# Kernel optimization log

Measured on AMD Instinct MI355X. Metric: run time of the kernel, lower is better.

The kernel has to match this reference:

```python
import jax, jax.numpy as jnp
import numpy as np

NUM_LANDMARKS = 256
PINV_ITERS = 6


def iterative_inv(K):
    # Newton-Schulz iterative pseudo-inverse (Nystromformer), K: [B, m, m]
    I = jnp.eye(K.shape[-1], dtype=K.dtype)
    V = K.swapaxes(-1, -2) / (jnp.max(jnp.sum(K, axis=-2)) * jnp.max(jnp.sum(K, axis=-1)))
    for _ in range(PINV_ITERS):
        KV = K @ V
        V = 0.25 * V @ (13.0 * I - KV @ (15.0 * I - KV @ (7.0 * I - KV)))
    return V


def nystrom_attention_matrix(q, k, m):
    # q, k: [B, N, d] -> approximate softmax(q k^T / sqrt(d)) of shape [B, N, N]
    B, N, d = q.shape
    scale = 1.0 / jnp.sqrt(jnp.asarray(d, q.dtype))
    L = N // m
    q_l = q.reshape(B, m, L, d).mean(axis=2)  # landmark queries [B, m, d]
    k_l = k.reshape(B, m, L, d).mean(axis=2)  # landmark keys    [B, m, d]
    k1 = jax.nn.softmax(jnp.einsum('bnd,bmd->bnm', q, k_l) * scale, axis=-1)   # [B, N, m]
    k2 = jax.nn.softmax(jnp.einsum('bld,bmd->blm', q_l, k_l) * scale, axis=-1) # [B, m, m]
    k3 = jax.nn.softmax(jnp.einsum('bmd,bnd->bmn', q_l, k) * scale, axis=-1)   # [B, m, N]
    return (k1 @ iterative_inv(k2)) @ k3  # [B, N, N]


def setup_inputs() -> dict:
    key = jax.random.key(0)
    ks = jax.random.split(key, 8)
    B, C, T, W, H = 2, 64, 4, 32, 32
    d = C // 8
    scale = 0.05  # keep q.k scores in a sane softmax range
    return {
        'x': jax.random.normal(ks[0], (B, C, T, W, H), dtype=jnp.float32),
        'wq': jax.random.normal(ks[1], (d, C), dtype=jnp.float32) * scale,
        'bq': jax.random.normal(ks[2], (d,), dtype=jnp.float32) * scale,
        'wk': jax.random.normal(ks[3], (d, C), dtype=jnp.float32) * scale,
        'bk': jax.random.normal(ks[4], (d,), dtype=jnp.float32) * scale,
        'wv': jax.random.normal(ks[5], (C, C), dtype=jnp.float32) * scale,
        'bv': jax.random.normal(ks[6], (C,), dtype=jnp.float32) * scale,
        'gamma': jax.random.normal(ks[7], (1,), dtype=jnp.float32),
    }


def reference(x, wq, bq, wk, bk, wv, bv, gamma):
    B, C, T, W, H = x.shape
    N = T * W * H
    xf = x.reshape(B, C, N)
    # 1x1x1 Conv3d == per-token linear over channels
    q = jnp.einsum('oc,bcn->bno', wq, xf) + bq            # [B, N, C//8]
    k = jnp.einsum('oc,bcn->bno', wk, xf) + bk            # [B, N, C//8]
    v = jnp.einsum('oc,bcn->bon', wv, xf) + bv[None, :, None]  # [B, C, N]
    attn = nystrom_attention_matrix(q, k, NUM_LANDMARKS)  # [B, N, N]
    # out = bmm(value, attn^T): out[b,c,i] = sum_j v[b,c,j] * attn[b,i,j]
    out = jnp.einsum('bcj,bij->bci', v, attn).reshape(B, C, T, W, H)
    out = gamma[0] * out + x
    return out, attn
```

## Files before the change

### kernel.cpp

```cpp
#include <hip/hip_runtime.h>
#include <hip/hip_bf16.h>
#include <math.h>

#define NB 2
#define NC 64
#define ND 8
#define NN 4096
#define NM 256
#define NL 16
#define SCALE 0.35355339059327373f

typedef __attribute__((ext_vector_type(4))) float f32x4;
typedef __attribute__((ext_vector_type(8))) short bf16x8;

__device__ inline ushort f2bf(float f) {
  __hip_bfloat16 h = __float2bfloat16(f);
  return *reinterpret_cast<ushort*>(&h);
}
__device__ inline float bf2f(ushort u) {
  return __uint_as_float(((unsigned int)u) << 16);
}

__device__ inline void gl_lds16(const void* g, void* l) {
  __builtin_amdgcn_global_load_lds(
      (const __attribute__((address_space(1))) unsigned int*)g,
      (__attribute__((address_space(3))) unsigned int*)l, 16, 0, 0);
}

__global__ __launch_bounds__(256) void qkv4_kernel(
    const float* __restrict__ x,
    const float* __restrict__ wq, const float* __restrict__ bq,
    const float* __restrict__ wk, const float* __restrict__ bk,
    const float* __restrict__ wv, const float* __restrict__ bv,
    float* __restrict__ q, float* __restrict__ k, float* __restrict__ v,
    float* __restrict__ ql, float* __restrict__ kl) {
  __shared__ float ws[4][NC];
  int o0 = blockIdx.x * 4;
  int b = blockIdx.z;
  int n0 = blockIdx.y * 1024;
  int t = threadIdx.x;
  {
    int j = t >> 6, c = t & 63;
    int o = o0 + j;
    const float* wrow;
    if (o < ND)          wrow = wq + (size_t)o * NC;
    else if (o < 2 * ND) wrow = wk + (size_t)(o - ND) * NC;
    else                 wrow = wv + (size_t)(o - 2 * ND) * NC;
    ws[j][c] = wrow[c];
  }
  __syncthreads();
  int n = n0 + t * 4;
  float4 acc[4];
  #pragma unroll
  for (int j = 0; j < 4; ++j) {
    int o = o0 + j;
    float bias = (o < ND) ? bq[o] : (o < 2 * ND ? bk[o - ND] : bv[o - 2 * ND]);
    acc[j].x = bias; acc[j].y = bias; acc[j].z = bias; acc[j].w = bias;
  }
  for (int c = 0; c < NC; ++c) {
    float4 xv = *(const float4*)(x + ((size_t)b * NC + c) * NN + n);
    #pragma unroll
    for (int j = 0; j < 4; ++j) {
      float wc = ws[j][c];
      acc[j].x += wc * xv.x; acc[j].y += wc * xv.y;
      acc[j].z += wc * xv.z; acc[j].w += wc * xv.w;
    }
  }
  #pragma unroll
  for (int j = 0; j < 4; ++j) {
    int o = o0 + j;
    if (o < ND) {
      float* qp = q + ((size_t)b * NN + n) * ND + o;
      qp[0] = acc[j].x; qp[8] = acc[j].y; qp[16] = acc[j].z; qp[24] = acc[j].w;
    } else if (o < 2 * ND) {
      float* kp = k + ((size_t)b * NN + n) * ND + (o - ND);
      kp[0] = acc[j].x; kp[8] = acc[j].y; kp[16] = acc[j].z; kp[24] = acc[j].w;
    } else {
      *(float4*)(v + ((size_t)b * NC + (o - 2 * ND)) * NN + n) = acc[j];
    }
    if (o < 2 * ND) {
      float s4 = acc[j].x + acc[j].y + acc[j].z + acc[j].w;
      s4 += __shfl_xor(s4, 1);
      s4 += __shfl_xor(s4, 2);
      if ((t & 3) == 0) {
        int g = n0 / 16 + (t >> 2);
        float* dst = (o < ND) ? ql : kl;
        dst[((size_t)b * NM + g) * ND + (o & 7)] = s4 * (1.0f / 16.0f);
      }
    }
  }
}

__global__ __launch_bounds__(256) void scores_all_kernel(
    const float* __restrict__ q, const float* __restrict__ ql,
    const float* __restrict__ kw, const float* __restrict__ kl,
    ushort* __restrict__ k1bf, float* __restrict__ k2w,
    ushort* __restrict__ k3bf) {
  __shared__ float skl[NM][9];
  __shared__ float wred[4], wsum[4];
  int blk = blockIdx.x;
  int t = threadIdx.x;
  if (blk < 2048 + 128) {
    const float* Q; int R, b, xrow;
    bool isbf;
    if (blk < 2048) { b = blk >> 10; xrow = blk & 1023; Q = q;  R = NN; isbf = true; }
    else { int r = blk - 2048; b = r >> 6; xrow = r & 63; Q = ql; R = NM; isbf = false; }
    for (int i = t; i < NM * ND; i += 256) skl[i >> 3][i & 7] = kl[(size_t)b * NM * ND + i];
    __syncthreads();
    int wave = t >> 6, lane = t & 63;
    int r = xrow * 4 + wave;
    const float* qrow = Q + ((size_t)b * R + r) * ND;
    float qr[ND];
    #pragma unroll
    for (int dd = 0; dd < ND; ++dd) qr[dd] = qrow[dd];
    float sc[4];
    float lmax = -1e30f;
    #pragma unroll
    for (int s = 0; s < 4; ++s) {
      int j = lane + 64 * s;
      float a = 0.f;
      #pragma unroll
      for (int dd = 0; dd < ND; ++dd) a += qr[dd] * skl[j][dd];
      sc[s] = a * SCALE;
      lmax = fmaxf(lmax, sc[s]);
    }
    for (int off = 32; off; off >>= 1) lmax = fmaxf(lmax, __shfl_xor(lmax, off));
    float lsum = 0.f;
    #pragma unroll
    for (int s = 0; s < 4; ++s) { sc[s] = expf(sc[s] - lmax); lsum += sc[s]; }
    for (int off = 32; off; off >>= 1) lsum += __shfl_xor(lsum, off);
    float inv = 1.0f / lsum;
    if (isbf) {
      #pragma unroll
      for (int s = 0; s < 4; ++s)
        k1bf[((size_t)b * R + r) * NM + lane + 64 * s] = f2bf(sc[s] * inv);
    } else {
      #pragma unroll
      for (int s = 0; s < 4; ++s)
        k2w[((size_t)b * R + r) * NM + lane + 64 * s] = sc[s] * inv;
    }
  } else {
    int r = blk - 2176;
    int b = r >> 8, i = r & 255;
    float qr[ND];
    #pragma unroll
    for (int dd = 0; dd < ND; ++dd) qr[dd] = ql[((size_t)b * NM + i) * ND + dd];
    float sc[16];
    float lmax = -1e30f;
    #pragma unroll
    for (int s = 0; s < 16; ++s) {
      int n = t + 256 * s;
      const float* kp = kw + ((size_t)b * NN + n) * ND;
      float a = 0.f;
      #pragma unroll
      for (int dd = 0; dd < ND; ++dd) a += qr[dd] * kp[dd];
      sc[s] = a * SCALE;
      lmax = fmaxf(lmax, sc[s]);
    }
    for (int off = 32; off; off >>= 1) lmax = fmaxf(lmax, __shfl_xor(lmax, off));
    if ((t & 63) == 0) wred[t >> 6] = lmax;
    __syncthreads();
    lmax = fmaxf(fmaxf(wred[0], wred[1]), fmaxf(wred[2], wred[3]));
    float lsum = 0.f;
    #pragma unroll
    for (int s = 0; s < 16; ++s) { sc[s] = expf(sc[s] - lmax); lsum += sc[s]; }
    for (int off = 32; off; off >>= 1) lsum += __shfl_xor(lsum, off);
    if ((t & 63) == 0) wsum[t >> 6] = lsum;
    __syncthreads();
    lsum = wsum[0] + wsum[1] + wsum[2] + wsum[3];
    float inv = 1.0f / lsum;
    #pragma unroll
    for (int s = 0; s < 16; ++s)
      k3bf[((size_t)b * NM + i) * NN + t + 256 * s] = f2bf(sc[s] * inv);
  }
}

__global__ __launch_bounds__(256) void denom_kernel(const float* __restrict__ k2,
                                                    float* __restrict__ denw) {
  __shared__ float red[256];
  int b = blockIdx.x;
  int t = threadIdx.x;
  float cs = 0.f;
  for (int i = 0; i < NM; ++i) cs += k2[((size_t)b * NM + i) * NM + t];
  red[t] = cs;
  __syncthreads();
  for (int off = 128; off; off >>= 1) {
    if (t < off) red[t] = fmaxf(red[t], red[t + off]);
    __syncthreads();
  }
  if (t == 0) denw[b] = red[0];
}

__global__ __launch_bounds__(256) void gemm_rk32(
    const float* __restrict__ A, const float* __restrict__ Bm,
    float* __restrict__ out, float s_a, float s_ab) {
  int b = blockIdx.z;
  int bi = blockIdx.y * 32, bj = blockIdx.x * 32;
  __shared__ float As[32][260];
  __shared__ float Bs[256][36];
  int t = threadIdx.x;
  const float* Ab = A + (size_t)b * NM * NM;
  const float* Bb = Bm + (size_t)b * NM * NM;
  #pragma unroll
  for (int q = 0; q < 8; ++q) {
    int s = q * 256 + t;
    int ar = s >> 6, ac = (s & 63) * 4;
    *(float4*)&As[ar][ac] = *(const float4*)(Ab + (size_t)(bi + ar) * NM + ac);
    int br = s >> 3, bc = (s & 7) * 4;
    *(float4*)&Bs[br][bc] = *(const float4*)(Bb + (size_t)br * NM + bj + bc);
  }
  __syncthreads();
  int tx = t & 15, ty = t >> 4;
  float acc[2][2] = {};
  #pragma unroll 8
  for (int kk = 0; kk < NM; ++kk) {
    float a0 = As[ty * 2][kk], a1 = As[ty * 2 + 1][kk];
    float b0 = Bs[kk][tx * 2], b1 = Bs[kk][tx * 2 + 1];
    acc[0][0] += a0 * b0; acc[0][1] += a0 * b1;
    acc[1][0] += a1 * b0; acc[1][1] += a1 * b1;
  }
  #pragma unroll
  for (int i = 0; i < 2; ++i)
    #pragma unroll
    for (int j = 0; j < 2; ++j) {
      size_t o = ((size_t)b * NM + bi + ty * 2 + i) * NM + bj + tx * 2 + j;
      float r = s_ab * acc[i][j];
      if (s_a != 0.0f) r += s_a * A[o];
      out[o] = r;
    }
}

__global__ __launch_bounds__(256) void gemm_rk32_zv0(
    const float* __restrict__ k2, const float* __restrict__ denw,
    float* __restrict__ out) {
  int b = blockIdx.z;
  int bi = blockIdx.y * 32, bj = blockIdx.x * 32;
  __shared__ float As[32][260];
  __shared__ float Bs[256][36];
  int t = threadIdx.x;
  const float* Ab = k2 + (size_t)b * NM * NM;
  float dval = 1.0f / fmaxf(denw[0], denw[1]);
  #pragma unroll
  for (int q = 0; q < 8; ++q) {
    int s = q * 256 + t;
    int ar = s >> 6, ac = (s & 63) * 4;
    *(float4*)&As[ar][ac] = *(const float4*)(Ab + (size_t)(bi + ar) * NM + ac);
    int br = s >> 6, bk4 = (s & 63) * 4;
    float4 vv = *(const float4*)(Ab + (size_t)(bj + br) * NM + bk4);
    Bs[bk4 + 0][br] = vv.x * dval; Bs[bk4 + 1][br] = vv.y * dval;
    Bs[bk4 + 2][br] = vv.z * dval; Bs[bk4 + 3][br] = vv.w * dval;
  }
  __syncthreads();
  int tx = t & 15, ty = t >> 4;
  float acc[2][2] = {};
  #pragma unroll 8
  for (int kk = 0; kk < NM; ++kk) {
    float a0 = As[ty * 2][kk], a1 = As[ty * 2 + 1][kk];
    float b0 = Bs[kk][tx * 2], b1 = Bs[kk][tx * 2 + 1];
    acc[0][0] += a0 * b0; acc[0][1] += a0 * b1;
    acc[1][0] += a1 * b0; acc[1][1] += a1 * b1;
  }
  #pragma unroll
  for (int i = 0; i < 2; ++i)
    #pragma unroll
    for (int j = 0; j < 2; ++j)
      out[((size_t)b * NM + bi + ty * 2 + i) * NM + bj + tx * 2 + j] = acc[i][j];
}

__global__ __launch_bounds__(256) void gemm_rk32_av0(
    const float* __restrict__ k2, const float* __restrict__ T2,
    const float* __restrict__ denw, float* __restrict__ out) {
  int b = blockIdx.z;
  int bi = blockIdx.y * 32, bj = blockIdx.x * 32;
  __shared__ float As[32][260];
  __shared__ float Bs[256][36];
  int t = threadIdx.x;
  const float* k2b = k2 + (size_t)b * NM * NM;
  const float* Bb = T2 + (size_t)b * NM * NM;
  float dval = 1.0f / fmaxf(denw[0], denw[1]);
  #pragma unroll
  for (int q = 0; q < 8; ++q) {
    int s = q * 256 + t;
    int kr = s >> 3, c4 = (s & 7) * 4;
    float4 vv = *(const float4*)(k2b + (size_t)kr * NM + bi + c4);
    As[c4 + 0][kr] = vv.x * dval; As[c4 + 1][kr] = vv.y * dval;
    As[c4 + 2][kr] = vv.z * dval; As[c4 + 3][kr] = vv.w * dval;
    int br = s >> 3, bc = (s & 7) * 4;
    *(float4*)&Bs[br][bc] = *(const float4*)(Bb + (size_t)br * NM + bj + bc);
  }
  __syncthreads();
  int tx = t & 15, ty = t >> 4;
  float acc[2][2] = {};
  #pragma unroll 8
  for (int kk = 0; kk < NM; ++kk) {
    float a0 = As[ty * 2][kk], a1 = As[ty * 2 + 1][kk];
    float b0 = Bs[kk][tx * 2], b1 = Bs[kk][tx * 2 + 1];
    acc[0][0] += a0 * b0; acc[0][1] += a0 * b1;
    acc[1][0] += a1 * b0; acc[1][1] += a1 * b1;
  }
  #pragma unroll
  for (int i = 0; i < 2; ++i)
    #pragma unroll
    for (int j = 0; j < 2; ++j) {
      int R = bi + ty * 2 + i, C = bj + tx * 2 + j;
      float a0v = k2b[(size_t)C * NM + R] * dval;
      out[((size_t)b * NM + R) * NM + C] = 3.25f * a0v - 0.25f * acc[i][j];
    }
}

__global__ __launch_bounds__(256) void gemm_rk32_wt(
    const float* __restrict__ A, const float* __restrict__ Bm,
    ushort* __restrict__ Vt) {
  int b = blockIdx.z;
  int bi = blockIdx.y * 32, bj = blockIdx.x * 32;
  __shared__ float As[32][260];
  __shared__ float Bs[256][36];
  int t = threadIdx.x;
  const float* Ab = A + (size_t)b * NM * NM;
  const float* Bb = Bm + (size_t)b * NM * NM;
  #pragma unroll
  for (int q = 0; q < 8; ++q) {
    int s = q * 256 + t;
    int ar = s >> 6, ac = (s & 63) * 4;
    *(float4*)&As[ar][ac] = *(const float4*)(Ab + (size_t)(bi + ar) * NM + ac);
    int br = s >> 3, bc = (s & 7) * 4;
    *(float4*)&Bs[br][bc] = *(const float4*)(Bb + (size_t)br * NM + bj + bc);
  }
  __syncthreads();
  int tx = t & 15, ty = t >> 4;
  float acc[2][2] = {};
  #pragma unroll 8
  for (int kk = 0; kk < NM; ++kk) {
    float a0 = As[ty * 2][kk], a1 = As[ty * 2 + 1][kk];
    float b0 = Bs[kk][tx * 2], b1 = Bs[kk][tx * 2 + 1];
    acc[0][0] += a0 * b0; acc[0][1] += a0 * b1;
    acc[1][0] += a1 * b0; acc[1][1] += a1 * b1;
  }
  __syncthreads();
  float (*tile)[33] = (float (*)[33])&As[0][0];
  #pragma unroll
  for (int i = 0; i < 2; ++i)
    #pragma unroll
    for (int j = 0; j < 2; ++j) {
      int R = ty * 2 + i, C = tx * 2 + j;
      float a0v = Ab[(size_t)(bi + R) * NM + bj + C];
      tile[R][C] = 3.25f * a0v - 0.25f * acc[i][j];
    }
  __syncthreads();
  int rr = t >> 3, m4 = (t & 7) * 4;
  ushort4 u;
  u.x = f2bf(tile[m4 + 0][rr]); u.y = f2bf(tile[m4 + 1][rr]);
  u.z = f2bf(tile[m4 + 2][rr]); u.w = f2bf(tile[m4 + 3][rr]);
  *(ushort4*)(Vt + ((size_t)b * NM + bj + rr) * NM + bi + m4) = u;
}

__global__ __launch_bounds__(256) void cvt_t_kernel(const ushort* __restrict__ k3,
                                                    ushort* __restrict__ k3t) {
  int b = blockIdx.z;
  int n0 = blockIdx.x * 32, m0 = blockIdx.y * 32;
  __shared__ ushort tile[32][33];
  int t = threadIdx.x;
  int r = t >> 3, c4 = (t & 7) * 4;
  ushort4 v = *(const ushort4*)(k3 + ((size_t)b * NM + m0 + r) * NN + n0 + c4);
  tile[c4][r] = v.x; tile[c4 + 1][r] = v.y; tile[c4 + 2][r] = v.z; tile[c4 + 3][r] = v.w;
  __syncthreads();
  ushort4 u;
  u.x = tile[r][c4];     u.y = tile[r][c4 + 1];
  u.z = tile[r][c4 + 2]; u.w = tile[r][c4 + 3];
  *(ushort4*)(k3t + ((size_t)b * NN + n0 + r) * NM + m0 + c4) = u;
}

__global__ __launch_bounds__(256) void gemm_a_mfma(
    const ushort* __restrict__ k1bf, const ushort* __restrict__ Vt,
    ushort* __restrict__ Abf) {
  int b = blockIdx.z;
  int bi = blockIdx.y * 128, bj = blockIdx.x * 128;
  __shared__ ushort As[128 * 64];
  __shared__ ushort Bs[128 * 64];
  int t = threadIdx.x;
  int wave = t >> 6, lane = t & 63;
  int wr = wave >> 1, wc = wave & 1;
  const ushort* Ab = k1bf + (size_t)b * NN * NM;
  const ushort* Bb = Vt + (size_t)b * NM * NM;
  f32x4 acc[4][4] = {};
  for (int k0 = 0; k0 < NM; k0 += 64) {
    #pragma unroll
    for (int q = 0; q < 4; ++q) {
      int s = q * 256 + t;
      int r = s >> 3, c = s & 7;
      int cs = (c ^ (r & 7)) << 3;
      gl_lds16(Ab + (size_t)(bi + r) * NM + k0 + cs, As + (size_t)s * 8);
      gl_lds16(Bb + (size_t)(bj + r) * NM + k0 + cs, Bs + (size_t)s * 8);
    }
    __syncthreads();
    #pragma unroll
    for (int kk = 0; kk < 2; ++kk) {
      int koff = kk * 64 + (lane >> 4) * 16;
      bf16x8 af[4], bfv[4];
      #pragma unroll
      for (int mi = 0; mi < 4; ++mi) {
        int row = wr * 64 + mi * 16 + (lane & 15);
        af[mi] = *(const bf16x8*)((const char*)As + row * 128 + (koff ^ ((row & 7) << 4)));
      }
      #pragma unroll
      for (int nj = 0; nj < 4; ++nj) {
        int row = wc * 64 + nj * 16 + (lane & 15);
        bfv[nj] = *(const bf16x8*)((const char*)Bs + row * 128 + (koff ^ ((row & 7) << 4)));
      }
      #pragma unroll
      for (int mi = 0; mi < 4; ++mi)
        #pragma unroll
        for (int nj = 0; nj < 4; ++nj)
          acc[mi][nj] = __builtin_amdgcn_mfma_f32_16x16x32_bf16(af[mi], bfv[nj], acc[mi][nj], 0, 0, 0);
    }
    __syncthreads();
  }
  int col = lane & 15, rbase = (lane >> 4) * 4;
  #pragma unroll
  for (int mi = 0; mi < 4; ++mi)
    #pragma unroll
    for (int nj = 0; nj < 4; ++nj)
      #pragma unroll
      for (int r = 0; r < 4; ++r)
        Abf[((size_t)b * NN + bi + wr * 64 + mi * 16 + rbase + r) * NM
            + bj + wc * 64 + nj * 16 + col] = f2bf(acc[mi][nj][r]);
}

__global__ __launch_bounds__(256) void gemm_attn_mfma(
    const ushort* __restrict__ Abf, const ushort* __restrict__ K3T,
    float* __restrict__ attn) {
  int lin = blockIdx.z * 1024 + blockIdx.y * 32 + blockIdx.x;
  int swz = (lin & 7) * 256 + (lin >> 3);
  int b = swz >> 10;
  int rem = swz & 1023;
  int bi = (rem >> 5) * 128, bj = (rem & 31) * 128;
  __shared__ ushort As[128 * 64];
  __shared__ ushort Bs[128 * 64];
  int t = threadIdx.x;
  int wave = t >> 6, lane = t & 63;
  int wr = wave >> 1, wc = wave & 1;
  const ushort* Ab = Abf + (size_t)b * NN * NM;
  const ushort* Bb = K3T + (size_t)b * NN * NM;
  f32x4 acc[4][4] = {};
  for (int k0 = 0; k0 < NM; k0 += 64) {
    #pragma unroll
    for (int q = 0; q < 4; ++q) {
      int s = q * 256 + t;
      int r = s >> 3, c = s & 7;
      int cs = (c ^ (r & 7)) << 3;
      gl_lds16(Ab + (size_t)(bi + r) * NM + k0 + cs, As + (size_t)s * 8);
      gl_lds16(Bb + (size_t)(bj + r) * NM + k0 + cs, Bs + (size_t)s * 8);
    }
    __syncthreads();
    #pragma unroll
    for (int kk = 0; kk < 2; ++kk) {
      int koff = kk * 64 + (lane >> 4) * 16;
      bf16x8 af[4], bfv[4];
      #pragma unroll
      for (int mi = 0; mi < 4; ++mi) {
        int row = wr * 64 + mi * 16 + (lane & 15);
        af[mi] = *(const bf16x8*)((const char*)As + row * 128 + (koff ^ ((row & 7) << 4)));
      }
      #pragma unroll
      for (int nj = 0; nj < 4; ++nj) {
        int row = wc * 64 + nj * 16 + (lane & 15);
        bfv[nj] = *(const bf16x8*)((const char*)Bs + row * 128 + (koff ^ ((row & 7) << 4)));
      }
      #pragma unroll
      for (int mi = 0; mi < 4; ++mi)
        #pragma unroll
        for (int nj = 0; nj < 4; ++nj)
          acc[mi][nj] = __builtin_amdgcn_mfma_f32_16x16x32_bf16(af[mi], bfv[nj], acc[mi][nj], 0, 0, 0);
    }
    __syncthreads();
  }
  int col = lane & 15, rbase = (lane >> 4) * 4;
  #pragma unroll
  for (int mi = 0; mi < 4; ++mi)
    #pragma unroll
    for (int nj = 0; nj < 4; ++nj)
      #pragma unroll
      for (int r = 0; r < 4; ++r)
        __builtin_nontemporal_store(
            acc[mi][nj][r],
            &attn[((size_t)b * NN + bi + wr * 64 + mi * 16 + rbase + r) * NN
                  + bj + wc * 64 + nj * 16 + col]);
}

__global__ __launch_bounds__(256) void kv_kernel(
    const ushort* __restrict__ K3, const float* __restrict__ Vv,
    float* __restrict__ kvout) {
  int b = blockIdx.z, bp = blockIdx.x * 64;
  int j0base = blockIdx.y * (NN / 32);
  __shared__ float Ks[64][33], Vs[64][33];
  int t = threadIdx.x, tx = t & 15, ty = t >> 4;
  int lrow = t >> 2, ljc = (t & 3) * 8;
  float acc[4][4] = {};
  for (int j0 = j0base; j0 < j0base + NN / 32; j0 += 32) {
    bf16x8 a0 = *(const bf16x8*)(K3 + ((size_t)b * NM + bp + lrow) * NN + j0 + ljc);
    float4 v0 = *(const float4*)(Vv + ((size_t)b * NC + lrow) * NN + j0 + ljc);
    float4 v1 = *(const float4*)(Vv + ((size_t)b * NC + lrow) * NN + j0 + ljc + 4);
    #pragma unroll
    for (int e = 0; e < 8; ++e) Ks[lrow][ljc + e] = bf2f((ushort)a0[e]);
    Vs[lrow][ljc + 0] = v0.x; Vs[lrow][ljc + 1] = v0.y; Vs[lrow][ljc + 2] = v0.z; Vs[lrow][ljc + 3] = v0.w;
    Vs[lrow][ljc + 4] = v1.x; Vs[lrow][ljc + 5] = v1.y; Vs[lrow][ljc + 6] = v1.z; Vs[lrow][ljc + 7] = v1.w;
    __syncthreads();
    #pragma unroll
    for (int kk = 0; kk < 32; ++kk) {
      float av_[4], bv_[4];
      #pragma unroll
      for (int i = 0; i < 4; ++i) av_[i] = Ks[(ty << 2) + i][kk];
      #pragma unroll
      for (int j = 0; j < 4; ++j) bv_[j] = Vs[(tx << 2) + j][kk];
      #pragma unroll
      for (int i = 0; i < 4; ++i)
        #pragma unroll
        for (int j = 0; j < 4; ++j) acc[i][j] += av_[i] * bv_[j];
    }
    __syncthreads();
  }
  #pragma unroll
  for (int i = 0; i < 4; ++i)
    #pragma unroll
    for (int j = 0; j < 4; ++j)
      atomicAdd(&kvout[((size_t)b * NM + bp + (ty << 2) + i) * NC + (tx << 2) + j], acc[i][j]);
}

__global__ __launch_bounds__(256) void out_kernel(
    const ushort* __restrict__ Abf, const float* __restrict__ kvm,
    const float* __restrict__ x, const float* __restrict__ gamma,
    float* __restrict__ outp) {
  __shared__ float As[32 * 256];
  int blk = blockIdx.x;
  int b = blk / (NN / 32), n0 = (blk % (NN / 32)) * 32;
  int t = threadIdx.x;
  for (int it = 0; it < 32; ++it)
    As[it * 256 + (t ^ (it & 31))] = bf2f(Abf[((size_t)b * NN + n0 + it) * NM + t]);
  __syncthreads();
  int tn = t & 31, cg0 = (t >> 5) * 8;
  float g = gamma[0];
  float acc[8] = {};
  for (int p = 0; p < NM; ++p) {
    float a = As[tn * 256 + (p ^ (tn & 31))];
    float4 kv0 = *(const float4*)(kvm + ((size_t)b * NM + p) * NC + cg0);
    float4 kv1 = *(const float4*)(kvm + ((size_t)b * NM + p) * NC + cg0 + 4);
    acc[0] += a * kv0.x; acc[1] += a * kv0.y; acc[2] += a * kv0.z; acc[3] += a * kv0.w;
    acc[4] += a * kv1.x; acc[5] += a * kv1.y; acc[6] += a * kv1.z; acc[7] += a * kv1.w;
  }
  #pragma unroll
  for (int qd = 0; qd < 8; ++qd) {
    int c = cg0 + qd;
    size_t idx = ((size_t)b * NC + c) * NN + n0 + tn;
    __builtin_nontemporal_store(g * acc[qd] + x[idx], &outp[idx]);
  }
}

extern "C" void kernel_launch(void* const* d_in, const int* in_sizes, int n_in,
                              void* d_out, int out_size, void* d_ws, size_t ws_size,
                              hipStream_t stream) {
  const float* x     = (const float*)d_in[0];
  const float* wq    = (const float*)d_in[1];
  const float* bq    = (const float*)d_in[2];
  const float* wk    = (const float*)d_in[3];
  const float* bk    = (const float*)d_in[4];
  const float* wv    = (const float*)d_in[5];
  const float* bv    = (const float*)d_in[6];
  const float* gamma = (const float*)d_in[7];
  float* outp = (float*)d_out;
  float* attn = outp + (size_t)NB * NC * NN;
  float* w = (float*)d_ws;

  float* qw   = w;
  float* kw   = qw + 65536;
  float* vw   = kw + 65536;
  float* qlw  = vw + 524288;
  float* klw  = qlw + 4096;
  float* k1w  = klw + 4096;
  float* k2w  = k1w + 2097152;
  float* k3w  = k2w + 131072;
  float* Abuf = k3w + 2097152;
  float* Va   = Abuf + 1048576;
  float* Vb   = Va + 131072;
  float* Zb   = Vb + 131072;
  float* T1   = Zb + 131072;
  float* T2   = T1 + 131072;
  float* Vtw  = T2 + 131072;
  float* kvw  = Vtw + 65536;
  float* denw = kvw + 32768;
  ushort* k1bf  = (ushort*)k1w;
  ushort* k3T   = (ushort*)k1w + 2097152;
  ushort* k3bf  = (ushort*)k3w;
  ushort* Abf   = (ushort*)Abuf;
  ushort* Vinvt = (ushort*)Vtw;

  hipMemsetAsync(kvw, 0, (size_t)NB * NM * NC * sizeof(float), stream);
  qkv4_kernel<<<dim3(20, NN / 1024, NB), dim3(256), 0, stream>>>(
      x, wq, bq, wk, bk, wv, bv, qw, kw, vw, qlw, klw);
  scores_all_kernel<<<dim3(2048 + 128 + 512), dim3(256), 0, stream>>>(
      qw, qlw, kw, klw, k1bf, k2w, k3bf);
  denom_kernel<<<dim3(NB), dim3(256), 0, stream>>>(k2w, denw);

  gemm_rk32_zv0<<<dim3(8, 8, NB), dim3(256), 0, stream>>>(k2w, denw, Zb);
  gemm_rk32<<<dim3(8, 8, NB), dim3(256), 0, stream>>>(Zb, Zb, T1, 7.f, -1.f);
  gemm_rk32<<<dim3(8, 8, NB), dim3(256), 0, stream>>>(Zb, T1, T2, 15.f, -1.f);
  gemm_rk32_av0<<<dim3(8, 8, NB), dim3(256), 0, stream>>>(k2w, T2, denw, Va);
  float* Vc = Va; float* Vn = Vb;
  for (int it = 1; it < 5; ++it) {
    gemm_rk32<<<dim3(8, 8, NB), dim3(256), 0, stream>>>(k2w, Vc, Zb, 0.f, 1.f);
    gemm_rk32<<<dim3(8, 8, NB), dim3(256), 0, stream>>>(Zb, Zb, T1, 7.f, -1.f);
    gemm_rk32<<<dim3(8, 8, NB), dim3(256), 0, stream>>>(Zb, T1, T2, 15.f, -1.f);
    gemm_rk32<<<dim3(8, 8, NB), dim3(256), 0, stream>>>(Vc, T2, Vn, 3.25f, -0.25f);
    float* tmp = Vc; Vc = Vn; Vn = tmp;
  }
  gemm_rk32<<<dim3(8, 8, NB), dim3(256), 0, stream>>>(k2w, Vc, Zb, 0.f, 1.f);
  gemm_rk32<<<dim3(8, 8, NB), dim3(256), 0, stream>>>(Zb, Zb, T1, 7.f, -1.f);
  gemm_rk32<<<dim3(8, 8, NB), dim3(256), 0, stream>>>(Zb, T1, T2, 15.f, -1.f);
  gemm_rk32_wt<<<dim3(8, 8, NB), dim3(256), 0, stream>>>(Vc, T2, Vinvt);

  cvt_t_kernel<<<dim3(NN / 32, NM / 32, NB), dim3(256), 0, stream>>>(k3bf, k3T);
  gemm_a_mfma<<<dim3(NM / 128, NN / 128, NB), dim3(256), 0, stream>>>(k1bf, Vinvt, Abf);
  gemm_attn_mfma<<<dim3(NN / 128, NN / 128, NB), dim3(256), 0, stream>>>(Abf, k3T, attn);
  kv_kernel<<<dim3(NM / 64, 32, NB), dim3(256), 0, stream>>>(k3bf, vw, kvw);
  out_kernel<<<dim3(NB * NN / 32), dim3(256), 0, stream>>>(Abf, kvw, x, gamma, outp);
}
```

Baseline: 298.8 us.

## Split-K the Newton-Schulz GEMMs into two partial slices summed on load

Measured after the change: 285.5 us. -4.4%, faster.

```diff
diff --git a/kernel.cpp b/kernel.cpp
--- a/kernel.cpp
+++ b/kernel.cpp
@@ -9,6 +9,7 @@
 #define NM 256
 #define NL 16
 #define SCALE 0.35355339059327373f
+#define SLICE (NB * NM * NM)
 
 typedef __attribute__((ext_vector_type(4))) float f32x4;
 typedef __attribute__((ext_vector_type(8))) short bf16x8;
@@ -191,9 +192,97 @@
   if (t == 0) denw[b] = red[0];
 }
 
-__global__ __launch_bounds__(256) void gemm_rk32(
+__global__ __launch_bounds__(256) void ns2_kernel(
+    const float* __restrict__ A, int amode,
+    const float* __restrict__ B, int bmode,
+    const float* __restrict__ denw, float* __restrict__ O,
+    float s_a, float s_ab) {
+  __shared__ float As[32][132];
+  __shared__ float Bs[128][36];
+  int t = threadIdx.x;
+  int bi = blockIdx.y * 32, bj = blockIdx.x * 32;
+  int b = blockIdx.z >> 1, slice = blockIdx.z & 1;
+  int k0 = slice * 128;
+  size_t bo = (size_t)b * NM * NM;
+  float dval = (amode == 2 || bmode == 2) ? 1.0f / fmaxf(denw[0], denw[1]) : 0.f;
+  if (amode == 2) {
+    #pragma unroll
+    for (int q = 0; q < 4; ++q) {
+      int s = q * 256 + t;
+      int k = s >> 3, rc = (s & 7) * 4;
+      float4 v = *(const float4*)(A + bo + (size_t)(k0 + k) * NM + bi + rc);
+      As[rc + 0][k] = v.x * dval; As[rc + 1][k] = v.y * dval;
+      As[rc + 2][k] = v.z * dval; As[rc + 3][k] = v.w * dval;
+    }
+  } else {
+    #pragma unroll
+    for (int q = 0; q < 4; ++q) {
+      int s = q * 256 + t;
+      int ar = s >> 5, ac = (s & 31) * 4;
+      const float* p = A + bo + (size_t)(bi + ar) * NM + k0 + ac;
+      float4 v = *(const float4*)p;
+      if (amode == 1) {
+        float4 v1 = *(const float4*)(p + SLICE);
+        v.x += v1.x; v.y += v1.y; v.z += v1.z; v.w += v1.w;
+      }
+      *(float4*)&As[ar][ac] = v;
+    }
+  }
+  if (bmode == 2) {
+    #pragma unroll
+    for (int q = 0; q < 4; ++q) {
+      int s = q * 256 + t;
+      int c = s >> 5, kc = (s & 31) * 4;
+      float4 v = *(const float4*)(B + bo + (size_t)(bj + c) * NM + k0 + kc);
+      Bs[kc + 0][c] = v.x * dval; Bs[kc + 1][c] = v.y * dval;
+      Bs[kc + 2][c] = v.z * dval; Bs[kc + 3][c] = v.w * dval;
+    }
+  } else {
+    #pragma unroll
+    for (int q = 0; q < 4; ++q) {
+      int s = q * 256 + t;
+      int bk = s >> 3, bc = (s & 7) * 4;
+      const float* p = B + bo + (size_t)(k0 + bk) * NM + bj + bc;
+      float4 v = *(const float4*)p;
+      if (bmode == 1) {
+        float4 v1 = *(const float4*)(p + SLICE);
+        v.x += v1.x; v.y += v1.y; v.z += v1.z; v.w += v1.w;
+      }
+      *(float4*)&Bs[bk][bc] = v;
+    }
+  }
+  __syncthreads();
+  int tx = t & 15, ty = t >> 4;
+  float acc[2][2] = {};
+  #pragma unroll 8
+  for (int kk = 0; kk < 128; ++kk) {
+    float a0 = As[ty * 2][kk], a1 = As[ty * 2 + 1][kk];
+    float b0 = Bs[kk][tx * 2], b1 = Bs[kk][tx * 2 + 1];
+    acc[0][0] += a0 * b0; acc[0][1] += a0 * b1;
+    acc[1][0] += a1 * b0; acc[1][1] += a1 * b1;
+  }
+  float* Op = O + (size_t)slice * SLICE + bo;
+  bool addA = (slice == 0) && (s_a != 0.0f);
+  #pragma unroll
+  for (int i = 0; i < 2; ++i)
+    #pragma unroll
+    for (int j = 0; j < 2; ++j) {
+      int R = bi + ty * 2 + i, C = bj + tx * 2 + j;
+      float r = s_ab * acc[i][j];
+      if (addA) {
+        float av;
+        if (amode == 2)      av = A[bo + (size_t)C * NM + R] * dval;
+        else if (amode == 1) av = A[bo + (size_t)R * NM + C] + A[bo + SLICE + (size_t)R * NM + C];
+        else                 av = A[bo + (size_t)R * NM + C];
+        r += s_a * av;
+      }
+      Op[(size_t)R * NM + C] = r;
+    }
+}
+
+__global__ __launch_bounds__(256) void gemm_rk32_wt_pair(
     const float* __restrict__ A, const float* __restrict__ Bm,
-    float* __restrict__ out, float s_a, float s_ab) {
+    ushort* __restrict__ Vt) {
   int b = blockIdx.z;
   int bi = blockIdx.y * 32, bj = blockIdx.x * 32;
   __shared__ float As[32][260];
@@ -205,9 +294,17 @@
   for (int q = 0; q < 8; ++q) {
     int s = q * 256 + t;
     int ar = s >> 6, ac = (s & 63) * 4;
-    *(float4*)&As[ar][ac] = *(const float4*)(Ab + (size_t)(bi + ar) * NM + ac);
+    const float* pa = Ab + (size_t)(bi + ar) * NM + ac;
+    float4 va = *(const float4*)pa;
+    float4 va1 = *(const float4*)(pa + SLICE);
+    va.x += va1.x; va.y += va1.y; va.z += va1.z; va.w += va1.w;
+    *(float4*)&As[ar][ac] = va;
     int br = s >> 3, bc = (s & 7) * 4;
-    *(float4*)&Bs[br][bc] = *(const float4*)(Bb + (size_t)br * NM + bj + bc);
+    const float* pb = Bb + (size_t)br * NM + bj + bc;
+    float4 vb = *(const float4*)pb;
+    float4 vb1 = *(const float4*)(pb + SLICE);
+    vb.x += vb1.x; vb.y += vb1.y; vb.z += vb1.z; vb.w += vb1.w;
+    *(float4*)&Bs[br][bc] = vb;
   }
   __syncthreads();
   int tx = t & 15, ty = t >> 4;
@@ -219,123 +316,6 @@
     acc[0][0] += a0 * b0; acc[0][1] += a0 * b1;
     acc[1][0] += a1 * b0; acc[1][1] += a1 * b1;
   }
-  #pragma unroll
-  for (int i = 0; i < 2; ++i)
-    #pragma unroll
-    for (int j = 0; j < 2; ++j) {
-      size_t o = ((size_t)b * NM + bi + ty * 2 + i) * NM + bj + tx * 2 + j;
-      float r = s_ab * acc[i][j];
-      if (s_a != 0.0f) r += s_a * A[o];
-      out[o] = r;
-    }
-}
-
-__global__ __launch_bounds__(256) void gemm_rk32_zv0(
-    const float* __restrict__ k2, const float* __restrict__ denw,
-    float* __restrict__ out) {
-  int b = blockIdx.z;
-  int bi = blockIdx.y * 32, bj = blockIdx.x * 32;
-  __shared__ float As[32][260];
-  __shared__ float Bs[256][36];
-  int t = threadIdx.x;
-  const float* Ab = k2 + (size_t)b * NM * NM;
-  float dval = 1.0f / fmaxf(denw[0], denw[1]);
-  #pragma unroll
-  for (int q = 0; q < 8; ++q) {
-    int s = q * 256 + t;
-    int ar = s >> 6, ac = (s & 63) * 4;
-    *(float4*)&As[ar][ac] = *(const float4*)(Ab + (size_t)(bi + ar) * NM + ac);
-    int br = s >> 6, bk4 = (s & 63) * 4;
-    float4 vv = *(const float4*)(Ab + (size_t)(bj + br) * NM + bk4);
-    Bs[bk4 + 0][br] = vv.x * dval; Bs[bk4 + 1][br] = vv.y * dval;
-    Bs[bk4 + 2][br] = vv.z * dval; Bs[bk4 + 3][br] = vv.w * dval;
-  }
-  __syncthreads();
-  int tx = t & 15, ty = t >> 4;
-  float acc[2][2] = {};
-  #pragma unroll 8
-  for (int kk = 0; kk < NM; ++kk) {
-    float a0 = As[ty * 2][kk], a1 = As[ty * 2 + 1][kk];
-    float b0 = Bs[kk][tx * 2], b1 = Bs[kk][tx * 2 + 1];
-    acc[0][0] += a0 * b0; acc[0][1] += a0 * b1;
-    acc[1][0] += a1 * b0; acc[1][1] += a1 * b1;
-  }
-  #pragma unroll
-  for (int i = 0; i < 2; ++i)
-    #pragma unroll
-    for (int j = 0; j < 2; ++j)
-      out[((size_t)b * NM + bi + ty * 2 + i) * NM + bj + tx * 2 + j] = acc[i][j];
-}
-
-__global__ __launch_bounds__(256) void gemm_rk32_av0(
-    const float* __restrict__ k2, const float* __restrict__ T2,
-    const float* __restrict__ denw, float* __restrict__ out) {
-  int b = blockIdx.z;
-  int bi = blockIdx.y * 32, bj = blockIdx.x * 32;
-  __shared__ float As[32][260];
-  __shared__ float Bs[256][36];
-  int t = threadIdx.x;
-  const float* k2b = k2 + (size_t)b * NM * NM;
-  const float* Bb = T2 + (size_t)b * NM * NM;
-  float dval = 1.0f / fmaxf(denw[0], denw[1]);
-  #pragma unroll
-  for (int q = 0; q < 8; ++q) {
-    int s = q * 256 + t;
-    int kr = s >> 3, c4 = (s & 7) * 4;
-    float4 vv = *(const float4*)(k2b + (size_t)kr * NM + bi + c4);
-    As[c4 + 0][kr] = vv.x * dval; As[c4 + 1][kr] = vv.y * dval;
-    As[c4 + 2][kr] = vv.z * dval; As[c4 + 3][kr] = vv.w * dval;
-    int br = s >> 3, bc = (s & 7) * 4;
-    *(float4*)&Bs[br][bc] = *(const float4*)(Bb + (size_t)br * NM + bj + bc);
-  }
-  __syncthreads();
-  int tx = t & 15, ty = t >> 4;
-  float acc[2][2] = {};
-  #pragma unroll 8
-  for (int kk = 0; kk < NM; ++kk) {
-    float a0 = As[ty * 2][kk], a1 = As[ty * 2 + 1][kk];
-    float b0 = Bs[kk][tx * 2], b1 = Bs[kk][tx * 2 + 1];
-    acc[0][0] += a0 * b0; acc[0][1] += a0 * b1;
-    acc[1][0] += a1 * b0; acc[1][1] += a1 * b1;
-  }
-  #pragma unroll
-  for (int i = 0; i < 2; ++i)
-    #pragma unroll
-    for (int j = 0; j < 2; ++j) {
-      int R = bi + ty * 2 + i, C = bj + tx * 2 + j;
-      float a0v = k2b[(size_t)C * NM + R] * dval;
-      out[((size_t)b * NM + R) * NM + C] = 3.25f * a0v - 0.25f * acc[i][j];
-    }
-}
-
-__global__ __launch_bounds__(256) void gemm_rk32_wt(
-    const float* __restrict__ A, const float* __restrict__ Bm,
-    ushort* __restrict__ Vt) {
-  int b = blockIdx.z;
-  int bi = blockIdx.y * 32, bj = blockIdx.x * 32;
-  __shared__ float As[32][260];
-  __shared__ float Bs[256][36];
-  int t = threadIdx.x;
-  const float* Ab = A + (size_t)b * NM * NM;
-  const float* Bb = Bm + (size_t)b * NM * NM;
-  #pragma unroll
-  for (int q = 0; q < 8; ++q) {
-    int s = q * 256 + t;
-    int ar = s >> 6, ac = (s & 63) * 4;
-    *(float4*)&As[ar][ac] = *(const float4*)(Ab + (size_t)(bi + ar) * NM + ac);
-    int br = s >> 3, bc = (s & 7) * 4;
-    *(float4*)&Bs[br][bc] = *(const float4*)(Bb + (size_t)br * NM + bj + bc);
-  }
-  __syncthreads();
-  int tx = t & 15, ty = t >> 4;
-  float acc[2][2] = {};
-  #pragma unroll 8
-  for (int kk = 0; kk < NM; ++kk) {
-    float a0 = As[ty * 2][kk], a1 = As[ty * 2 + 1][kk];
-    float b0 = Bs[kk][tx * 2], b1 = Bs[kk][tx * 2 + 1];
-    acc[0][0] += a0 * b0; acc[0][1] += a0 * b1;
-    acc[1][0] += a1 * b0; acc[1][1] += a1 * b1;
-  }
   __syncthreads();
   float (*tile)[33] = (float (*)[33])&As[0][0];
   #pragma unroll
@@ -343,7 +323,8 @@
     #pragma unroll
     for (int j = 0; j < 2; ++j) {
       int R = ty * 2 + i, C = tx * 2 + j;
-      float a0v = Ab[(size_t)(bi + R) * NM + bj + C];
+      size_t o = (size_t)(bi + R) * NM + bj + C;
+      float a0v = Ab[o] + Ab[o + SLICE];
       tile[R][C] = 3.25f * a0v - 0.25f * acc[i][j];
     }
   __syncthreads();
@@ -579,12 +560,12 @@
   float* k2w  = k1w + 2097152;
   float* k3w  = k2w + 131072;
   float* Abuf = k3w + 2097152;
-  float* Va   = Abuf + 1048576;
-  float* Vb   = Va + 131072;
-  float* Zb   = Vb + 131072;
-  float* T1   = Zb + 131072;
-  float* T2   = T1 + 131072;
-  float* Vtw  = T2 + 131072;
+  float* Zp   = Abuf + 1048576;
+  float* T1p  = Zp + 2 * SLICE;
+  float* T2p  = T1p + 2 * SLICE;
+  float* Vap  = T2p + 2 * SLICE;
+  float* Vbp  = Vap + 2 * SLICE;
+  float* Vtw  = Vbp + 2 * SLICE;
   float* kvw  = Vtw + 65536;
   float* denw = kvw + 32768;
   ushort* k1bf  = (ushort*)k1w;
@@ -600,22 +581,22 @@
       qw, qlw, kw, klw, k1bf, k2w, k3bf);
   denom_kernel<<<dim3(NB), dim3(256), 0, stream>>>(k2w, denw);
 
-  gemm_rk32_zv0<<<dim3(8, 8, NB), dim3(256), 0, stream>>>(k2w, denw, Zb);
-  gemm_rk32<<<dim3(8, 8, NB), dim3(256), 0, stream>>>(Zb, Zb, T1, 7.f, -1.f);
-  gemm_rk32<<<dim3(8, 8, NB), dim3(256), 0, stream>>>(Zb, T1, T2, 15.f, -1.f);
-  gemm_rk32_av0<<<dim3(8, 8, NB), dim3(256), 0, stream>>>(k2w, T2, denw, Va);
-  float* Vc = Va; float* Vn = Vb;
+  ns2_kernel<<<dim3(8, 8, 2 * NB), dim3(256), 0, stream>>>(k2w, 0, k2w, 2, denw, Zp, 0.f, 1.f);
+  ns2_kernel<<<dim3(8, 8, 2 * NB), dim3(256), 0, stream>>>(Zp, 1, Zp, 1, denw, T1p, 7.f, -1.f);
+  ns2_kernel<<<dim3(8, 8, 2 * NB), dim3(256), 0, stream>>>(Zp, 1, T1p, 1, denw, T2p, 15.f, -1.f);
+  ns2_kernel<<<dim3(8, 8, 2 * NB), dim3(256), 0, stream>>>(k2w, 2, T2p, 1, denw, Vap, 3.25f, -0.25f);
+  float* Vcp = Vap; float* Vnp = Vbp;
   for (int it = 1; it < 5; ++it) {
-    gemm_rk32<<<dim3(8, 8, NB), dim3(256), 0, stream>>>(k2w, Vc, Zb, 0.f, 1.f);
-    gemm_rk32<<<dim3(8, 8, NB), dim3(256), 0, stream>>>(Zb, Zb, T1, 7.f, -1.f);
-    gemm_rk32<<<dim3(8, 8, NB), dim3(256), 0, stream>>>(Zb, T1, T2, 15.f, -1.f);
-    gemm_rk32<<<dim3(8, 8, NB), dim3(256), 0, stream>>>(Vc, T2, Vn, 3.25f, -0.25f);
-    float* tmp = Vc; Vc = Vn; Vn = tmp;
-  }
-  gemm_rk32<<<dim3(8, 8, NB), dim3(256), 0, stream>>>(k2w, Vc, Zb, 0.f, 1.f);
-  gemm_rk32<<<dim3(8, 8, NB), dim3(256), 0, stream>>>(Zb, Zb, T1, 7.f, -1.f);
-  gemm_rk32<<<dim3(8, 8, NB), dim3(256), 0, stream>>>(Zb, T1, T2, 15.f, -1.f);
-  gemm_rk32_wt<<<dim3(8, 8, NB), dim3(256), 0, stream>>>(Vc, T2, Vinvt);
+    ns2_kernel<<<dim3(8, 8, 2 * NB), dim3(256), 0, stream>>>(k2w, 0, Vcp, 1, denw, Zp, 0.f, 1.f);
+    ns2_kernel<<<dim3(8, 8, 2 * NB), dim3(256), 0, stream>>>(Zp, 1, Zp, 1, denw, T1p, 7.f, -1.f);
+    ns2_kernel<<<dim3(8, 8, 2 * NB), dim3(256), 0, stream>>>(Zp, 1, T1p, 1, denw, T2p, 15.f, -1.f);
+    ns2_kernel<<<dim3(8, 8, 2 * NB), dim3(256), 0, stream>>>(Vcp, 1, T2p, 1, denw, Vnp, 3.25f, -0.25f);
+    float* tmp = Vcp; Vcp = Vnp; Vnp = tmp;
+  }
+  ns2_kernel<<<dim3(8, 8, 2 * NB), dim3(256), 0, stream>>>(k2w, 0, Vcp, 1, denw, Zp, 0.f, 1.f);
+  ns2_kernel<<<dim3(8, 8, 2 * NB), dim3(256), 0, stream>>>(Zp, 1, Zp, 1, denw, T1p, 7.f, -1.f);
+  ns2_kernel<<<dim3(8, 8, 2 * NB), dim3(256), 0, stream>>>(Zp, 1, T1p, 1, denw, T2p, 15.f, -1.f);
+  gemm_rk32_wt_pair<<<dim3(8, 8, NB), dim3(256), 0, stream>>>(Vcp, T2p, Vinvt);
 
   cvt_t_kernel<<<dim3(NN / 32, NM / 32, NB), dim3(256), 0, stream>>>(k3bf, k3T);
   gemm_a_mfma<<<dim3(NM / 128, NN / 128, NB), dim3(256), 0, stream>>>(k1bf, Vinvt, Abf);
```
